# Optimization experiments

Hardware: AMD Instinct MI355X
Metric: run time of the kernel (lower is better)

## Reference

```python
import jax, jax.numpy as jnp
import numpy as np

SEQ, BATCH, HID = 4096, 32, 512


def setup_inputs() -> dict:
    key = jax.random.key(0)
    ks = jax.random.split(key, 7)
    s = 1.0 / np.sqrt(HID)
    return {
        "x0": jax.random.normal(ks[0], (SEQ, BATCH, 1), dtype=jnp.float32),
        "W_ih": jax.random.uniform(ks[1], (4 * HID, 1), jnp.float32, -s, s),
        "W_hh": jax.random.uniform(ks[2], (4 * HID, HID), jnp.float32, -s, s),
        "b_ih": jax.random.uniform(ks[3], (4 * HID,), jnp.float32, -s, s),
        "b_hh": jax.random.uniform(ks[4], (4 * HID,), jnp.float32, -s, s),
        "W_lin": jax.random.uniform(ks[5], (1, HID), jnp.float32, -s, s),
        "b_lin": jax.random.uniform(ks[6], (1,), jnp.float32, -s, s),
    }


def _lstm(x0, W_ih, W_hh, b_ih, b_hh):
    # x0: (T, B, 1). Precompute input contribution to gates for all steps.
    x_proj = jnp.einsum("tbi,gi->tbg", x0, W_ih) + (b_ih + b_hh)  # (T, B, 4H)
    T, B, _ = x_proj.shape
    H = W_hh.shape[1]
    h0 = jnp.zeros((B, H), x0.dtype)
    c0 = jnp.zeros((B, H), x0.dtype)

    def step(carry, xp):
        h, c = carry
        gates = xp + h @ W_hh.T  # (B, 4H)
        i, f, g, o = jnp.split(gates, 4, axis=-1)  # torch gate order i,f,g,o
        i = jax.nn.sigmoid(i)
        f = jax.nn.sigmoid(f)
        g = jnp.tanh(g)
        o = jax.nn.sigmoid(o)
        c = f * c + i * g
        h = o * jnp.tanh(c)
        return (h, c), h

    _, hs = jax.lax.scan(step, (h0, c0), x_proj)  # hs: (T, B, H)
    return hs


def reference(x0, W_ih, W_hh, b_ih, b_hh, W_lin, b_lin):
    hs = _lstm(x0, W_ih, W_hh, b_ih, b_hh)            # (T, B, H)
    y = jnp.einsum("tbh,oh->tbo", hs, W_lin) + b_lin  # (T, B, 1)
    return y + x0                                      # residual add
```

## Files before the change

### kernel.cpp

```cpp
#include <hip/hip_runtime.h>
#include <stdint.h>

#define T_STEPS 4096
#define BATCH 32
#define HID 512
#define GROUPS 8
#define BLK_THREADS 1024
#define NBLOCKS 256
#define BSLOT_DW 256
#define SLOT_DW (BATCH * BSLOT_DW)
#define TAG_STRIDE 16

typedef _Float16 h2_t __attribute__((ext_vector_type(2)));
typedef uint32_t u32x8 __attribute__((ext_vector_type(8)));
typedef uint32_t u32x16 __attribute__((ext_vector_type(16)));

__device__ inline uint32_t pack_h2(float a, float b) {
  h2_t v;
  v.x = (_Float16)a;
  v.y = (_Float16)b;
  return __builtin_bit_cast(uint32_t, v);
}

__device__ inline float fdot2(uint32_t a, uint32_t b, float c) {
  return __builtin_amdgcn_fdot2(__builtin_bit_cast(h2_t, a),
                                __builtin_bit_cast(h2_t, b), c, false);
}

__device__ inline uint64_t uni64(const void* p) {
  uint32_t lo = __builtin_amdgcn_readfirstlane((uint32_t)(uintptr_t)p);
  uint32_t hi = __builtin_amdgcn_readfirstlane((uint32_t)((uintptr_t)p >> 32));
  return ((uint64_t)hi << 32) | lo;
}

__device__ inline void kinv() {
  asm volatile("s_dcache_inv" ::: "memory");
}
__device__ inline u32x8 sload8(uint64_t p) {
  u32x8 v;
  asm volatile("s_load_dwordx8 %0, %1, 0x0\n\ts_waitcnt lgkmcnt(0)"
               : "=&s"(v) : "s"(p) : "memory");
  return v;
}
__device__ inline void sload32(uint64_t p, u32x16* a, u32x16* b) {
  asm volatile("s_load_dwordx16 %0, %2, 0x0\n\t"
               "s_load_dwordx16 %1, %2, 0x40\n\t"
               "s_waitcnt lgkmcnt(0)"
               : "=&s"(*a), "=&s"(*b) : "s"(p) : "memory");
}

__device__ inline float sigf(float x) { return 1.0f / (1.0f + __expf(-x)); }
__device__ inline float tanh_fast(float x) {
  float a = fabsf(x);
  float e = __expf(-2.0f * a);
  float r = (1.0f - e) / (1.0f + e);
  return copysignf(r, x);
}

__global__ __launch_bounds__(BLK_THREADS)
void lstm_onepoll2(const float* __restrict__ x0,
                   const float* __restrict__ W_ih,
                   const float* __restrict__ W_hh,
                   const float* __restrict__ b_ih,
                   const float* __restrict__ b_hh,
                   const float* __restrict__ W_lin,
                   const float* __restrict__ b_lin,
                   float* __restrict__ y,
                   uint32_t* __restrict__ h_ex,
                   uint32_t* __restrict__ tags,
                   int* __restrict__ claim)
{
  __shared__ float x0_lds[T_STEPS];
  __shared__ float ylds[T_STEPS];
  __shared__ float gacc[2][256];
  __shared__ int hflag[8];
  __shared__ int s_bg;

  const int tid = threadIdx.x;

  if (tid == 0) {
    uint32_t xcc;
    asm volatile("s_getreg_b32 %0, hwreg(HW_REG_XCC_ID)" : "=s"(xcc));
    xcc &= 7;
    int slot = atomicAdd(claim + xcc * 16, 1);
    s_bg = (slot < 32) ? (int)(((4 * xcc + (slot >> 3)) << 3) | (slot & 7))
                       : -1;
  }
  __syncthreads();
  if (s_bg < 0) return;
  const int b  = s_bg >> 3;
  const int g  = s_bg & 7;
  const int u0 = g * 64;
  const int wv = tid >> 6;
  const int rg = wv >> 3;
  const int cs = wv & 7;
  const int l  = tid & 63;

  uint32_t w0[32], w1[32];
  {
    const int r0 = 128 * rg + l;
    const int r1 = r0 + 64;
    const int R0 = (r0 >> 6) * HID + u0 + (r0 & 63);
    const int R1 = (r1 >> 6) * HID + u0 + (r1 & 63);
    const float2* p0 = (const float2*)(W_hh + (size_t)R0 * HID + 64 * cs);
    const float2* p1 = (const float2*)(W_hh + (size_t)R1 * HID + 64 * cs);
#pragma unroll
    for (int k = 0; k < 32; ++k) {
      float2 a = p0[k], c = p1[k];
      w0[k] = pack_h2(a.x, a.y);
      w1[k] = pack_h2(c.x, c.y);
    }
  }
  for (int i = tid; i < T_STEPS; i += BLK_THREADS) {
    x0_lds[i] = x0[i * BATCH + b];
    ylds[i] = 0.f;
  }
  if (tid < 256) { gacc[0][tid] = 0.f; gacc[1][tid] = 0.f; }
  if (tid < 8) hflag[tid] = 0;

  float c_state = 0.f;
  float wih_[4] = {0.f, 0.f, 0.f, 0.f}, bs_[4] = {0.f, 0.f, 0.f, 0.f};
  float wlin_u = 0.f, blin = 0.f;
  if (tid < 64) {
#pragma unroll
    for (int j = 0; j < 4; ++j) {
      int R = j * HID + u0 + tid;
      wih_[j] = W_ih[R];
      bs_[j] = b_ih[R] + b_hh[R];
    }
    wlin_u = W_lin[u0 + tid];
    blin = b_lin[0];
  }

  uint32_t* tags_b = tags + b * TAG_STRIDE;
  const uint64_t tagu = uni64(tags_b);
  uint32_t* hb0 = h_ex + (size_t)b * BSLOT_DW;
  const uint64_t dpu[2] = { uni64(hb0 + 32 * cs),
                            uni64(hb0 + SLOT_DW + 32 * cs) };
  uint32_t* pub01[2] = { hb0 + 32 * g, hb0 + SLOT_DW + 32 * g };

  __syncthreads();

  int dead = 0;
  for (int t = 0; t < T_STEPS; ++t) {
    const int sl = t & 1, ns = sl ^ 1;

    if (wv == 15) {
      if (!dead) {
        int guard = 0;
        for (;;) {
          kinv();
          u32x8 tg = sload8(tagu);
          if (l == 0) {
#pragma unroll
            for (int i = 0; i < 8; ++i)
              ((volatile int*)hflag)[i] = (int)tg[i];
          }
          bool ok = ((int)tg[0] >= t) & ((int)tg[1] >= t) &
                    ((int)tg[2] >= t) & ((int)tg[3] >= t) &
                    ((int)tg[4] >= t) & ((int)tg[5] >= t) &
                    ((int)tg[6] >= t) & ((int)tg[7] >= t);
          if (ok) break;
          if (++guard > (1 << 16)) { dead = 1; break; }
          __builtin_amdgcn_s_sleep(1);
        }
        if (dead && l == 0) {
#pragma unroll
          for (int i = 0; i < 8; ++i)
            ((volatile int*)hflag)[i] = 0x7fffffff;
        }
      }
    } else {
      int guard = 0;
      while (((volatile int*)hflag)[cs] < t) {
        if (++guard > (1 << 18)) break;
        __builtin_amdgcn_s_sleep(1);
      }
    }

    u32x16 h0_, h1_;
    sload32(dpu[sl], &h0_, &h1_);

    float acc0a = 0.f, acc0b = 0.f, acc1a = 0.f, acc1b = 0.f;
#pragma unroll
    for (int k = 0; k < 16; ++k) {
      acc0a = fdot2(w0[k], h0_[k], acc0a);
      acc1a = fdot2(w1[k], h0_[k], acc1a);
      acc0b = fdot2(w0[16 + k], h1_[k], acc0b);
      acc1b = fdot2(w1[16 + k], h1_[k], acc1b);
    }
    atomicAdd(&gacc[sl][128 * rg + l], acc0a + acc0b);
    atomicAdd(&gacc[sl][128 * rg + 64 + l], acc1a + acc1b);
    __syncthreads();

    if (tid < 64) {
      const float xv = x0_lds[t];
      float gi = gacc[sl][tid]       + xv * wih_[0] + bs_[0];
      float gf = gacc[sl][tid + 64]  + xv * wih_[1] + bs_[1];
      float gg = gacc[sl][tid + 128] + xv * wih_[2] + bs_[2];
      float go = gacc[sl][tid + 192] + xv * wih_[3] + bs_[3];
      float si = sigf(gi), sf = sigf(gf), tg_ = tanh_fast(gg), so = sigf(go);
      c_state = sf * c_state + si * tg_;
      float h = so * tanh_fast(c_state);

      ((_Float16*)pub01[ns])[tid] = (_Float16)h;
      asm volatile("s_waitcnt vmcnt(0)" ::: "memory");
      if (tid == 0) tags_b[g] = (uint32_t)(t + 1);

      gacc[sl][tid] = 0.f;
      gacc[sl][tid + 64] = 0.f;
      gacc[sl][tid + 128] = 0.f;
      gacc[sl][tid + 192] = 0.f;

      float p = wlin_u * h;
#pragma unroll
      for (int m = 32; m >= 1; m >>= 1) p += __shfl_xor(p, m, 64);
      if (tid == 0) ylds[t] = p;
    }
  }

  __syncthreads();
  for (int i = tid; i < T_STEPS; i += BLK_THREADS) {
    float val = ylds[i];
    if (g == 0) val += blin + x0_lds[i];
    unsafeAtomicAdd(&y[i * BATCH + b], val);
  }
}

extern "C" void kernel_launch(void* const* d_in, const int* in_sizes, int n_in,
                              void* d_out, int out_size, void* d_ws, size_t ws_size,
                              hipStream_t stream) {
  const float* x0    = (const float*)d_in[0];
  const float* W_ih  = (const float*)d_in[1];
  const float* W_hh  = (const float*)d_in[2];
  const float* b_ih  = (const float*)d_in[3];
  const float* b_hh  = (const float*)d_in[4];
  const float* W_lin = (const float*)d_in[5];
  const float* b_lin = (const float*)d_in[6];
  float* y = (float*)d_out;

  uint32_t* h_ex = (uint32_t*)d_ws;
  uint32_t* tags = h_ex + 2 * SLOT_DW;
  int* claim     = (int*)(tags + BATCH * TAG_STRIDE);
  const size_t init_bytes =
      (size_t)(2 * SLOT_DW + BATCH * TAG_STRIDE) * sizeof(uint32_t)
      + 8 * 16 * sizeof(int);

  (void)hipMemsetAsync(d_ws, 0, init_bytes, stream);
  (void)hipMemsetAsync(d_out, 0, (size_t)out_size * sizeof(float), stream);

  hipLaunchKernelGGL(lstm_onepoll2, dim3(NBLOCKS), dim3(BLK_THREADS), 0, stream,
                     x0, W_ih, W_hh, b_ih, b_hh, W_lin, b_lin, y, h_ex, tags,
                     claim);
}
```

Baseline: 15.74 ms.

## Fetch hidden state via vector loads with readlane broadcast and 8-slot ring

Replaces the per-wave scalar s_load of the shared hidden-state slice with one per-lane global_load_dword, broadcasting each packed half2 via readlane. The exchange buffer becomes an 8-slot ring, with a buffer_inv issued every 4 steps by the polling wave instead of relying on the scalar cache path. Publication now packs two fp16 values per dword using a shuffle. The aim is to cut scalar-cache invalidation latency on the critical inter-block handoff. The cost is vector-memory latency plus 32 readlanes per step, and the ring relies on stale-line reuse being safe with infrequent invalidation.

```diff
diff --git a/kernel.cpp b/kernel.cpp
--- a/kernel.cpp
+++ b/kernel.cpp
@@ -9,11 +9,11 @@
 #define NBLOCKS 256
 #define BSLOT_DW 256
 #define SLOT_DW (BATCH * BSLOT_DW)
+#define NSLOT 8
 #define TAG_STRIDE 16
 
 typedef _Float16 h2_t __attribute__((ext_vector_type(2)));
 typedef uint32_t u32x8 __attribute__((ext_vector_type(8)));
-typedef uint32_t u32x16 __attribute__((ext_vector_type(16)));
 
 __device__ inline uint32_t pack_h2(float a, float b) {
   h2_t v;
@@ -36,17 +36,20 @@
 __device__ inline void kinv() {
   asm volatile("s_dcache_inv" ::: "memory");
 }
+__device__ inline void binv() {
+  asm volatile("buffer_inv" ::: "memory");
+}
 __device__ inline u32x8 sload8(uint64_t p) {
   u32x8 v;
   asm volatile("s_load_dwordx8 %0, %1, 0x0\n\ts_waitcnt lgkmcnt(0)"
                : "=&s"(v) : "s"(p) : "memory");
   return v;
 }
-__device__ inline void sload32(uint64_t p, u32x16* a, u32x16* b) {
-  asm volatile("s_load_dwordx16 %0, %2, 0x0\n\t"
-               "s_load_dwordx16 %1, %2, 0x40\n\t"
-               "s_waitcnt lgkmcnt(0)"
-               : "=&s"(*a), "=&s"(*b) : "s"(p) : "memory");
+__device__ inline uint32_t vload_dw(const uint32_t* p) {
+  uint32_t v;
+  asm volatile("global_load_dword %0, %1, off\n\ts_waitcnt vmcnt(0)"
+               : "=v"(v) : "v"(p) : "memory");
+  return v;
 }
 
 __device__ inline float sigf(float x) { return 1.0f / (1.0f + __expf(-x)); }
@@ -58,17 +61,17 @@
 }
 
 __global__ __launch_bounds__(BLK_THREADS)
-void lstm_onepoll2(const float* __restrict__ x0,
-                   const float* __restrict__ W_ih,
-                   const float* __restrict__ W_hh,
-                   const float* __restrict__ b_ih,
-                   const float* __restrict__ b_hh,
-                   const float* __restrict__ W_lin,
-                   const float* __restrict__ b_lin,
-                   float* __restrict__ y,
-                   uint32_t* __restrict__ h_ex,
-                   uint32_t* __restrict__ tags,
-                   int* __restrict__ claim)
+void lstm_vecdata(const float* __restrict__ x0,
+                  const float* __restrict__ W_ih,
+                  const float* __restrict__ W_hh,
+                  const float* __restrict__ b_ih,
+                  const float* __restrict__ b_hh,
+                  const float* __restrict__ W_lin,
+                  const float* __restrict__ b_lin,
+                  float* __restrict__ y,
+                  uint32_t* __restrict__ h_ex,
+                  uint32_t* __restrict__ tags,
+                  int* __restrict__ claim)
 {
   __shared__ float x0_lds[T_STEPS];
   __shared__ float ylds[T_STEPS];
@@ -134,18 +137,19 @@
 
   uint32_t* tags_b = tags + b * TAG_STRIDE;
   const uint64_t tagu = uni64(tags_b);
-  uint32_t* hb0 = h_ex + (size_t)b * BSLOT_DW;
-  const uint64_t dpu[2] = { uni64(hb0 + 32 * cs),
-                            uni64(hb0 + SLOT_DW + 32 * cs) };
-  uint32_t* pub01[2] = { hb0 + 32 * g, hb0 + SLOT_DW + 32 * g };
+  uint32_t* hb = h_ex + (size_t)b * BSLOT_DW;
+  uint32_t* fet_base = hb + 32 * cs + (l & 31);
+  uint32_t* pub_base = hb + 32 * g;
 
   __syncthreads();
 
   int dead = 0;
   for (int t = 0; t < T_STEPS; ++t) {
-    const int sl = t & 1, ns = sl ^ 1;
+    const int sl = t & (NSLOT - 1);
+    const int ns = (t + 1) & (NSLOT - 1);
 
     if (wv == 15) {
+      if ((t & 3) == 0) binv();
       if (!dead) {
         int guard = 0;
         for (;;) {
@@ -178,39 +182,41 @@
       }
     }
 
-    u32x16 h0_, h1_;
-    sload32(dpu[sl], &h0_, &h1_);
+    uint32_t hval = vload_dw(fet_base + sl * SLOT_DW);
 
     float acc0a = 0.f, acc0b = 0.f, acc1a = 0.f, acc1b = 0.f;
 #pragma unroll
-    for (int k = 0; k < 16; ++k) {
-      acc0a = fdot2(w0[k], h0_[k], acc0a);
-      acc1a = fdot2(w1[k], h0_[k], acc1a);
-      acc0b = fdot2(w0[16 + k], h1_[k], acc0b);
-      acc1b = fdot2(w1[16 + k], h1_[k], acc1b);
-    }
-    atomicAdd(&gacc[sl][128 * rg + l], acc0a + acc0b);
-    atomicAdd(&gacc[sl][128 * rg + 64 + l], acc1a + acc1b);
+    for (int k = 0; k < 32; k += 2) {
+      uint32_t ha = __builtin_amdgcn_readlane(hval, k);
+      uint32_t hb2 = __builtin_amdgcn_readlane(hval, k + 1);
+      acc0a = fdot2(w0[k], ha, acc0a);
+      acc1a = fdot2(w1[k], ha, acc1a);
+      acc0b = fdot2(w0[k + 1], hb2, acc0b);
+      acc1b = fdot2(w1[k + 1], hb2, acc1b);
+    }
+    atomicAdd(&gacc[t & 1][128 * rg + l], acc0a + acc0b);
+    atomicAdd(&gacc[t & 1][128 * rg + 64 + l], acc1a + acc1b);
     __syncthreads();
 
     if (tid < 64) {
       const float xv = x0_lds[t];
-      float gi = gacc[sl][tid]       + xv * wih_[0] + bs_[0];
-      float gf = gacc[sl][tid + 64]  + xv * wih_[1] + bs_[1];
-      float gg = gacc[sl][tid + 128] + xv * wih_[2] + bs_[2];
-      float go = gacc[sl][tid + 192] + xv * wih_[3] + bs_[3];
+      float gi = gacc[t & 1][tid]       + xv * wih_[0] + bs_[0];
+      float gf = gacc[t & 1][tid + 64]  + xv * wih_[1] + bs_[1];
+      float gg = gacc[t & 1][tid + 128] + xv * wih_[2] + bs_[2];
+      float go = gacc[t & 1][tid + 192] + xv * wih_[3] + bs_[3];
       float si = sigf(gi), sf = sigf(gf), tg_ = tanh_fast(gg), so = sigf(go);
       c_state = sf * c_state + si * tg_;
       float h = so * tanh_fast(c_state);
 
-      ((_Float16*)pub01[ns])[tid] = (_Float16)h;
+      float hn = __shfl_down(h, 1, 64);
+      if ((tid & 1) == 0) pub_base[ns * SLOT_DW + (tid >> 1)] = pack_h2(h, hn);
       asm volatile("s_waitcnt vmcnt(0)" ::: "memory");
       if (tid == 0) tags_b[g] = (uint32_t)(t + 1);
 
-      gacc[sl][tid] = 0.f;
-      gacc[sl][tid + 64] = 0.f;
-      gacc[sl][tid + 128] = 0.f;
-      gacc[sl][tid + 192] = 0.f;
+      gacc[t & 1][tid] = 0.f;
+      gacc[t & 1][tid + 64] = 0.f;
+      gacc[t & 1][tid + 128] = 0.f;
+      gacc[t & 1][tid + 192] = 0.f;
 
       float p = wlin_u * h;
 #pragma unroll
@@ -240,16 +246,16 @@
   float* y = (float*)d_out;
 
   uint32_t* h_ex = (uint32_t*)d_ws;
-  uint32_t* tags = h_ex + 2 * SLOT_DW;
+  uint32_t* tags = h_ex + NSLOT * SLOT_DW;
   int* claim     = (int*)(tags + BATCH * TAG_STRIDE);
   const size_t init_bytes =
-      (size_t)(2 * SLOT_DW + BATCH * TAG_STRIDE) * sizeof(uint32_t)
+      (size_t)(NSLOT * SLOT_DW + BATCH * TAG_STRIDE) * sizeof(uint32_t)
       + 8 * 16 * sizeof(int);
 
   (void)hipMemsetAsync(d_ws, 0, init_bytes, stream);
   (void)hipMemsetAsync(d_out, 0, (size_t)out_size * sizeof(float), stream);
 
-  hipLaunchKernelGGL(lstm_onepoll2, dim3(NBLOCKS), dim3(BLK_THREADS), 0, stream,
+  hipLaunchKernelGGL(lstm_vecdata, dim3(NBLOCKS), dim3(BLK_THREADS), 0, stream,
                      x0, W_ih, W_hh, b_ih, b_hh, W_lin, b_lin, y, h_ex, tags,
                      claim);
 }
```

Result: slower. 16.17 ms (+2.7%).
